# Kernel optimization log

Hardware: AMD Instinct MI355X
Metric: run time of the kernel (lower is better)

The kernel has to match this reference:

```python
import jax, jax.numpy as jnp
import numpy as np

D_MODEL = 1024
N_EXPERTS = 16
TOP_K = 2
D_FF = 512      # per-expert SwiGLU hidden size
D_FF_SHARED = 1024
N_TOKENS = 4096


def setup_inputs() -> dict:
    key = jax.random.key(0)
    ks = jax.random.split(key, 9)
    s_in = 1.0 / np.sqrt(D_MODEL)
    s_ff = 1.0 / np.sqrt(D_FF)
    s_fs = 1.0 / np.sqrt(D_FF_SHARED)
    return {
        "hidden_states": jax.random.normal(ks[0], (N_TOKENS, D_MODEL), jnp.float32),
        "Wg": jax.random.normal(ks[1], (D_MODEL, N_EXPERTS), jnp.float32) * s_in,
        "w1": jax.random.normal(ks[2], (N_EXPERTS, D_MODEL, D_FF), jnp.float32) * s_in,
        "w3": jax.random.normal(ks[3], (N_EXPERTS, D_MODEL, D_FF), jnp.float32) * s_in,
        "w2": jax.random.normal(ks[4], (N_EXPERTS, D_FF, D_MODEL), jnp.float32) * s_ff,
        "ws1": jax.random.normal(ks[5], (D_MODEL, D_FF_SHARED), jnp.float32) * s_in,
        "ws3": jax.random.normal(ks[6], (D_MODEL, D_FF_SHARED), jnp.float32) * s_in,
        "ws2": jax.random.normal(ks[7], (D_FF_SHARED, D_MODEL), jnp.float32) * s_fs,
        "capacity": 1024,
    }


def reference(hidden_states, Wg, w1, w3, w2, ws1, ws3, ws2, capacity):
    T, d = hidden_states.shape
    E = Wg.shape[1]
    C = capacity

    # --- router: softmax in fp32, top-k, renormalize (norm_topk_prob=True) ---
    logits = hidden_states @ Wg                                  # [T, E]
    probs = jax.nn.softmax(logits.astype(jnp.float32), axis=-1)
    topw, topi = jax.lax.top_k(probs, TOP_K)                     # [T, K]
    topw = topw / jnp.sum(topw, axis=-1, keepdims=True)
    topw = topw.astype(hidden_states.dtype)

    # --- dispatch: flatten (token, k) pairs, compute slot within expert buffer ---
    flat_e = topi.reshape(-1)                                    # [T*K] expert id
    flat_t = jnp.repeat(jnp.arange(T), TOP_K)                    # [T*K] source token
    flat_w = topw.reshape(-1)                                    # [T*K]
    oh = jax.nn.one_hot(flat_e, E, dtype=jnp.int32)              # [T*K, E]
    # exclusive position of each pair within its expert's buffer
    pos = jnp.sum((jnp.cumsum(oh, axis=0) - 1) * oh, axis=-1)    # [T*K]
    keep = pos < C
    slot = jnp.where(keep, flat_e * C + pos, E * C)              # dropped -> dummy row

    buf = jnp.zeros((E * C + 1, d), hidden_states.dtype)
    buf = buf.at[slot].set(hidden_states[flat_t])
    xb = buf[: E * C].reshape(E, C, d)                           # [E, C, d]

    # --- per-expert SwiGLU MLP (grouped matmuls) ---
    h = jax.nn.silu(jnp.einsum("ecd,edf->ecf", xb, w1)) * jnp.einsum("ecd,edf->ecf", xb, w3)
    ob = jnp.einsum("ecf,efd->ecd", h, w2).reshape(E * C, d)     # [E*C, d]

    # --- weighted combine: gather expert outputs, scatter-add into token rows ---
    gathered = ob[jnp.minimum(slot, E * C - 1)]                  # [T*K, d]
    y = gathered * (flat_w * keep.astype(flat_w.dtype))[:, None]
    final = jnp.zeros_like(hidden_states).at[flat_t].add(y)

    # --- shared expert (dense SwiGLU over all tokens) ---
    sh = jax.nn.silu(hidden_states @ ws1) * (hidden_states @ ws3)
    final = final + sh @ ws2
    return final
```

## Files before the change

kernel.cpp:

```cpp
#include <hip/hip_runtime.h>
#include <stdint.h>

#define TT 4096
#define DM 1024
#define NE 16
#define DFF 512
#define DFS 1024
#define CAP 1024

typedef unsigned short u16;
typedef __bf16 bf16x8 __attribute__((ext_vector_type(8)));
typedef float f32x4 __attribute__((ext_vector_type(4)));

typedef __attribute__((address_space(1))) void as1_void;
typedef __attribute__((address_space(3))) void as3_void;

__device__ __forceinline__ u16 f2bf(float f) {
  union { float f; uint32_t u; } v; v.f = f;
  uint32_t u = v.u;
  u += 0x7fffu + ((u >> 16) & 1u);
  return (u16)(u >> 16);
}

__device__ __forceinline__ float bf2f(u16 b) {
  union { uint32_t u; float f; } v; v.u = ((uint32_t)b) << 16;
  return v.f;
}

__device__ __forceinline__ void gl2lds16(const void* g, void* l) {
  __builtin_amdgcn_global_load_lds(
      (as1_void*)(uintptr_t)g,
      (as3_void*)(uint32_t)(uintptr_t)l,
      16, 0, 0);
}

__global__ __launch_bounds__(256) void k_prep(
    const float* __restrict__ x, const float* __restrict__ Wg,
    const float* __restrict__ w1, const float* __restrict__ w3,
    const float* __restrict__ w2, const float* __restrict__ ws1,
    const float* __restrict__ ws3, const float* __restrict__ ws2,
    u16* __restrict__ hbf,
    u16* __restrict__ w1t, u16* __restrict__ w3t, u16* __restrict__ w2t,
    u16* __restrict__ ws1t, u16* __restrict__ ws3t, u16* __restrict__ ws2t,
    int* __restrict__ counts, int* __restrict__ tok_slot,
    int* __restrict__ tslot, float* __restrict__ tw) {
  __shared__ __align__(16) char smraw[18496];
  __shared__ int pick_e[32];
  __shared__ int base_sh[16];
  const int bid = blockIdx.x;
  const int tid = threadIdx.x;

  if (bid < 256) {
    float (*red)[16][17] = (float(*)[16][17])smraw;
    float (*lg)[17] = (float(*)[17])(smraw + 17408);
    int tl = tid >> 4, kp = tid & 15;
    int t = bid * 16 + tl;
    const float* xr = x + (size_t)t * DM + kp * 64;
    u16* hr = hbf + (size_t)t * DM + kp * 64;
    float acc[16];
#pragma unroll
    for (int e = 0; e < 16; ++e) acc[e] = 0.f;
#pragma unroll 4
    for (int i = 0; i < 16; ++i) {
      float4 xv = *(const float4*)(xr + i * 4);
      ushort4 o;
      o.x = f2bf(xv.x); o.y = f2bf(xv.y); o.z = f2bf(xv.z); o.w = f2bf(xv.w);
      *(ushort4*)(hr + i * 4) = o;
      const float* wgr = Wg + (size_t)(kp * 64 + i * 4) * NE;
#pragma unroll
      for (int q = 0; q < 4; ++q) {
        float xq = (q == 0) ? xv.x : (q == 1) ? xv.y : (q == 2) ? xv.z : xv.w;
        float4 a = *(const float4*)(wgr + q * NE);
        float4 b = *(const float4*)(wgr + q * NE + 4);
        float4 c = *(const float4*)(wgr + q * NE + 8);
        float4 d = *(const float4*)(wgr + q * NE + 12);
        acc[0] += xq * a.x;  acc[1] += xq * a.y;  acc[2] += xq * a.z;  acc[3] += xq * a.w;
        acc[4] += xq * b.x;  acc[5] += xq * b.y;  acc[6] += xq * b.z;  acc[7] += xq * b.w;
        acc[8] += xq * c.x;  acc[9] += xq * c.y;  acc[10] += xq * c.z; acc[11] += xq * c.w;
        acc[12] += xq * d.x; acc[13] += xq * d.y; acc[14] += xq * d.z; acc[15] += xq * d.w;
      }
    }
#pragma unroll
    for (int e = 0; e < 16; ++e) red[tl][kp][e] = acc[e];
    __syncthreads();
    float logit = 0.f;
#pragma unroll
    for (int p = 0; p < 16; ++p) logit += red[tl][p][kp];
    lg[tl][kp] = logit;
    __syncthreads();
    if (kp == 0) {
      float b0 = -1e30f; int i0 = 0;
#pragma unroll
      for (int i = 0; i < NE; ++i) { float v = lg[tl][i]; if (v > b0) { b0 = v; i0 = i; } }
      float b1 = -1e30f; int i1 = 0;
#pragma unroll
      for (int i = 0; i < NE; ++i) { if (i == i0) continue; float v = lg[tl][i]; if (v > b1) { b1 = v; i1 = i; } }
      float ex = __expf(b1 - b0);
      float w0 = 1.f / (1.f + ex);
      float w1v = 1.f - w0;
      pick_e[2 * tl] = i0;
      pick_e[2 * tl + 1] = i1;
      tw[2 * t] = w0; tw[2 * t + 1] = w1v;
    }
    __syncthreads();
    if (tid < 16) {
      int c = 0;
#pragma unroll
      for (int j = 0; j < 32; ++j) c += (pick_e[j] == tid) ? 1 : 0;
      int base = 0;
      if (c > 0) base = atomicAdd(&counts[tid], c);
      base_sh[tid] = base;
    }
    __syncthreads();
    if (kp == 0) {
#pragma unroll
      for (int kk = 0; kk < 2; ++kk) {
        int idx = 2 * tl + kk;
        int e = pick_e[idx];
        int rank = 0;
        for (int j = 0; j < idx; ++j) rank += (pick_e[j] == e) ? 1 : 0;
        int p = base_sh[e] + rank;
        int s = -1;
        if (p < CAP) { s = e * CAP + p; tok_slot[s] = t; }
        tslot[2 * t + kk] = s;
      }
    }
    return;
  }

  int tb = bid - 256;
  int z = tb >> 8, xy = tb & 255;
  const float* ip; u16* op; int R, C;
  if (z < 16)      { ip = w1 + (size_t)z * DM * DFF;       op = w1t + (size_t)z * DM * DFF;       R = DM;  C = DFF; }
  else if (z < 32) { int e = z - 16; ip = w3 + (size_t)e * DM * DFF; op = w3t + (size_t)e * DM * DFF; R = DM;  C = DFF; }
  else if (z < 48) { int e = z - 32; ip = w2 + (size_t)e * DFF * DM; op = w2t + (size_t)e * DFF * DM; R = DFF; C = DM; }
  else if (z == 48){ ip = ws1; op = ws1t; R = DM;  C = DFS; }
  else if (z == 49){ ip = ws3; op = ws3t; R = DM;  C = DFS; }
  else             { ip = ws2; op = ws2t; R = DFS; C = DM; }

  int c0 = (xy & 15) * 64, r0 = (xy >> 4) * 64;
  if (c0 >= C || r0 >= R) return;

  float (*tile)[65] = (float(*)[65])smraw;
  int tx = tid & 15, ty = tid >> 4;
#pragma unroll
  for (int j = 0; j < 4; ++j) {
    int r = ty + 16 * j;
    float4 v = *(const float4*)&ip[(size_t)(r0 + r) * C + c0 + tx * 4];
    *(float4*)&tile[r][tx * 4] = v;
  }
  __syncthreads();
#pragma unroll
  for (int j = 0; j < 4; ++j) {
    int c = ty + 16 * j;
    ushort4 o;
    o.x = f2bf(tile[tx * 4 + 0][c]);
    o.y = f2bf(tile[tx * 4 + 1][c]);
    o.z = f2bf(tile[tx * 4 + 2][c]);
    o.w = f2bf(tile[tx * 4 + 3][c]);
    *(ushort4*)&op[(size_t)(c0 + c) * R + r0 + tx * 4] = o;
  }
}

#define FRAG(BUF, ROW, CC)                                                       \
  (*(const bf16x8*)&BUF[(ROW) * 64 + ((((CC) * 4 + lq) ^ ((ROW) & 7)) << 3)])

__global__ __launch_bounds__(128) void k_up(
    const u16* __restrict__ hbf,
    const u16* __restrict__ ws1t, const u16* __restrict__ ws3t,
    const u16* __restrict__ w1t, const u16* __restrict__ w3t,
    u16* __restrict__ hs, u16* __restrict__ hexp,
    const int* __restrict__ counts, const int* __restrict__ tok_slot) {
  const int bid = blockIdx.x;
  const int tid = threadIdx.x;
  const u16* B1p; const u16* B3p; u16* Cp;
  int m0, n0, N;
  int e = -1, cnt = 0;
  if (bid < 512) {
    m0 = (bid >> 4) * 128; n0 = (bid & 15) * 64;
    B1p = ws1t; B3p = ws3t; Cp = hs; N = DFS;
  } else {
    int r = bid - 512;
    e = r >> 6; int q = r & 63;
    m0 = (q >> 3) * 128; n0 = (q & 7) * 64;
    cnt = counts[e]; if (cnt > CAP) cnt = CAP;
    if (m0 >= cnt) return;
    B1p = w1t + (size_t)e * (DFF * DM);
    B3p = w3t + (size_t)e * (DFF * DM);
    Cp = hexp + (size_t)e * (CAP * DFF);
    N = DFF;
  }

  __shared__ __align__(16) u16 As[128 * 64];
  __shared__ __align__(16) u16 Bs1[64 * 64];
  __shared__ __align__(16) u16 Bs3[64 * 64];

  uint32_t aoff[8], boff[4];
#pragma unroll
  for (int j = 0; j < 8; ++j) {
    int L = tid + 128 * j;
    int row = L >> 3;
    int c = (L & 7) ^ (row & 7);
    int gr;
    if (e >= 0) {
      int rr = m0 + row;
      gr = (rr < cnt) ? tok_slot[e * CAP + rr] : 0;
    } else {
      gr = m0 + row;
    }
    aoff[j] = (uint32_t)gr * DM + c * 8;
  }
#pragma unroll
  for (int j = 0; j < 4; ++j) {
    int L = tid + 128 * j;
    int row = L >> 3;
    int c = (L & 7) ^ (row & 7);
    boff[j] = (uint32_t)(n0 + row) * DM + c * 8;
  }

  const int lane = tid & 63;
  const int wv = tid >> 6;
  const int wr = wv * 64;
  const int lr = lane & 15;
  const int lq = lane >> 4;

  f32x4 acc1[4][4], acc3[4][4];
#pragma unroll
  for (int i = 0; i < 4; ++i)
#pragma unroll
    for (int j = 0; j < 4; ++j) {
      acc1[i][j] = (f32x4){0.f, 0.f, 0.f, 0.f};
      acc3[i][j] = (f32x4){0.f, 0.f, 0.f, 0.f};
    }

  for (int k0 = 0; k0 < DM; k0 += 64) {
    __syncthreads();
#pragma unroll
    for (int j = 0; j < 8; ++j) gl2lds16(hbf + aoff[j] + k0, &As[(size_t)(tid + 128 * j) * 8]);
#pragma unroll
    for (int j = 0; j < 4; ++j) gl2lds16(B1p + boff[j] + k0, &Bs1[(size_t)(tid + 128 * j) * 8]);
#pragma unroll
    for (int j = 0; j < 4; ++j) gl2lds16(B3p + boff[j] + k0, &Bs3[(size_t)(tid + 128 * j) * 8]);
    __syncthreads();
#pragma unroll
    for (int cc = 0; cc < 2; ++cc) {
      bf16x8 af[4], bf1[4], bf3[4];
#pragma unroll
      for (int i = 0; i < 4; ++i) af[i] = FRAG(As, wr + i * 16 + lr, cc);
#pragma unroll
      for (int j = 0; j < 4; ++j) {
        bf1[j] = FRAG(Bs1, j * 16 + lr, cc);
        bf3[j] = FRAG(Bs3, j * 16 + lr, cc);
      }
#pragma unroll
      for (int i = 0; i < 4; ++i)
#pragma unroll
        for (int j = 0; j < 4; ++j) {
          acc1[i][j] = __builtin_amdgcn_mfma_f32_16x16x32_bf16(af[i], bf1[j], acc1[i][j], 0, 0, 0);
          acc3[i][j] = __builtin_amdgcn_mfma_f32_16x16x32_bf16(af[i], bf3[j], acc3[i][j], 0, 0, 0);
        }
    }
  }

#pragma unroll
  for (int i = 0; i < 4; ++i)
#pragma unroll
    for (int r = 0; r < 4; ++r) {
      int row = m0 + wr + i * 16 + lq * 4 + r;
      u16* crow = Cp + (size_t)row * N;
#pragma unroll
      for (int j = 0; j < 4; ++j) {
        float v1 = acc1[i][j][r];
        float v3 = acc3[i][j][r];
        float h = (v1 / (1.f + __expf(-v1))) * v3;
        crow[n0 + j * 16 + lr] = f2bf(h);
      }
    }
}

__global__ __launch_bounds__(128) void k_down(
    const u16* __restrict__ hs, const u16* __restrict__ ws2t,
    const u16* __restrict__ hexp, const u16* __restrict__ w2t,
    float* __restrict__ out, u16* __restrict__ ob,
    const int* __restrict__ counts) {
  const int bid = blockIdx.x;
  const int tid = threadIdx.x;
  const u16* Ap; const u16* Bp;
  int m0, n0, K, e = -1;
  if (bid < 512) {
    m0 = (bid >> 4) * 128; n0 = (bid & 15) * 64;
    Ap = hs; Bp = ws2t; K = DFS;
  } else {
    int r = bid - 512;
    e = r >> 7; int q = r & 127;
    m0 = (q >> 4) * 128; n0 = (q & 15) * 64;
    int cnt = counts[e]; if (cnt > CAP) cnt = CAP;
    if (m0 >= cnt) return;
    Ap = hexp + (size_t)e * (CAP * DFF);
    Bp = w2t + (size_t)e * (DM * DFF);
    K = DFF;
  }

  __shared__ __align__(16) u16 As[128 * 64];
  __shared__ __align__(16) u16 Bs[64 * 64];

  uint32_t aoff[8], boff[4];
#pragma unroll
  for (int j = 0; j < 8; ++j) {
    int L = tid + 128 * j;
    int row = L >> 3;
    int c = (L & 7) ^ (row & 7);
    aoff[j] = (uint32_t)(m0 + row) * K + c * 8;
  }
#pragma unroll
  for (int j = 0; j < 4; ++j) {
    int L = tid + 128 * j;
    int row = L >> 3;
    int c = (L & 7) ^ (row & 7);
    boff[j] = (uint32_t)(n0 + row) * K + c * 8;
  }

  const int lane = tid & 63;
  const int wv = tid >> 6;
  const int wr = wv * 64;
  const int lr = lane & 15;
  const int lq = lane >> 4;

  f32x4 acc[4][4];
#pragma unroll
  for (int i = 0; i < 4; ++i)
#pragma unroll
    for (int j = 0; j < 4; ++j) acc[i][j] = (f32x4){0.f, 0.f, 0.f, 0.f};

  for (int k0 = 0; k0 < K; k0 += 64) {
    __syncthreads();
#pragma unroll
    for (int j = 0; j < 8; ++j) gl2lds16(Ap + aoff[j] + k0, &As[(size_t)(tid + 128 * j) * 8]);
#pragma unroll
    for (int j = 0; j < 4; ++j) gl2lds16(Bp + boff[j] + k0, &Bs[(size_t)(tid + 128 * j) * 8]);
    __syncthreads();
#pragma unroll
    for (int cc = 0; cc < 2; ++cc) {
      bf16x8 af[4], bfr[4];
#pragma unroll
      for (int i = 0; i < 4; ++i) af[i] = FRAG(As, wr + i * 16 + lr, cc);
#pragma unroll
      for (int j = 0; j < 4; ++j) bfr[j] = FRAG(Bs, j * 16 + lr, cc);
#pragma unroll
      for (int i = 0; i < 4; ++i)
#pragma unroll
        for (int j = 0; j < 4; ++j)
          acc[i][j] = __builtin_amdgcn_mfma_f32_16x16x32_bf16(af[i], bfr[j], acc[i][j], 0, 0, 0);
    }
  }

  if (e < 0) {
#pragma unroll
    for (int i = 0; i < 4; ++i)
#pragma unroll
      for (int r = 0; r < 4; ++r) {
        int row = m0 + wr + i * 16 + lq * 4 + r;
        float* orow = out + (size_t)row * DM;
#pragma unroll
        for (int j = 0; j < 4; ++j)
          orow[n0 + j * 16 + lr] = acc[i][j][r];
      }
  } else {
    u16* obase = ob + (size_t)e * CAP * DM;
#pragma unroll
    for (int i = 0; i < 4; ++i)
#pragma unroll
      for (int r = 0; r < 4; ++r) {
        int row = m0 + wr + i * 16 + lq * 4 + r;
        u16* orow = obase + (size_t)row * DM;
#pragma unroll
        for (int j = 0; j < 4; ++j)
          orow[n0 + j * 16 + lr] = f2bf(acc[i][j][r]);
      }
  }
}

__global__ __launch_bounds__(256) void k_combine(
    float* __restrict__ out, const u16* __restrict__ ob,
    const int* __restrict__ tslot, const float* __restrict__ tw) {
  int t = blockIdx.x;
  int c = threadIdx.x * 4;
  int s0 = tslot[2 * t], s1 = tslot[2 * t + 1];
  float w0 = tw[2 * t], w1 = tw[2 * t + 1];
  float4 v = *(float4*)&out[(size_t)t * DM + c];
  if (s0 >= 0) {
    ushort4 o = *(const ushort4*)&ob[(size_t)s0 * DM + c];
    v.x += w0 * bf2f(o.x); v.y += w0 * bf2f(o.y);
    v.z += w0 * bf2f(o.z); v.w += w0 * bf2f(o.w);
  }
  if (s1 >= 0) {
    ushort4 o = *(const ushort4*)&ob[(size_t)s1 * DM + c];
    v.x += w1 * bf2f(o.x); v.y += w1 * bf2f(o.y);
    v.z += w1 * bf2f(o.z); v.w += w1 * bf2f(o.w);
  }
  *(float4*)&out[(size_t)t * DM + c] = v;
}

extern "C" void kernel_launch(void* const* d_in, const int* in_sizes, int n_in,
                              void* d_out, int out_size, void* d_ws, size_t ws_size,
                              hipStream_t stream) {
  (void)in_sizes; (void)n_in; (void)out_size; (void)ws_size;
  const float* x   = (const float*)d_in[0];
  const float* Wg  = (const float*)d_in[1];
  const float* w1  = (const float*)d_in[2];
  const float* w3  = (const float*)d_in[3];
  const float* w2  = (const float*)d_in[4];
  const float* ws1 = (const float*)d_in[5];
  const float* ws3 = (const float*)d_in[6];
  const float* ws2 = (const float*)d_in[7];
  float* out = (float*)d_out;
  char* ws = (char*)d_ws;

  u16* hbf   = (u16*)(ws + 0);
  u16* w1t   = (u16*)(ws + 8388608);
  u16* w3t   = (u16*)(ws + 25165824);
  u16* w2t   = (u16*)(ws + 41943040);
  u16* ws1t  = (u16*)(ws + 58720256);
  u16* ws3t  = (u16*)(ws + 60817408);
  u16* ws2t  = (u16*)(ws + 62914560);
  u16* hs    = (u16*)(ws + 65011712);
  u16* hexp  = (u16*)(ws + 73400320);
  int* counts    = (int*)(ws + 90177536);
  int* tok_slot  = (int*)(ws + 90177792);
  int* tslot     = (int*)(ws + 90243328);
  float* tw      = (float*)(ws + 90276096);
  u16* ob    = (u16*)(ws + 0);

  hipMemsetAsync(counts, 0, NE * sizeof(int), stream);

  k_prep<<<dim3(256 + 51 * 256), dim3(256), 0, stream>>>(
      x, Wg, w1, w3, w2, ws1, ws3, ws2,
      hbf, w1t, w3t, w2t, ws1t, ws3t, ws2t,
      counts, tok_slot, tslot, tw);

  k_up<<<dim3(512 + NE * 64), dim3(128), 0, stream>>>(
      hbf, ws1t, ws3t, w1t, w3t, hs, hexp, counts, tok_slot);

  k_down<<<dim3(512 + NE * 128), dim3(128), 0, stream>>>(
      hs, ws2t, hexp, w2t, out, ob, counts);

  k_combine<<<dim3(TT), dim3(256), 0, stream>>>(out, ob, tslot, tw);
}
```

Before: 319.9 us.

## Double-buffer LDS tiles in up and down expert GEMM kernels

Both the gate/up GEMM and the down GEMM now keep two LDS buffers per operand. The next K tile's global-to-LDS loads are issued before computing on the current tile, so memory latency overlaps MFMA work and one barrier per iteration is removed. This doubles shared memory use, which may cut occupancy: the up kernel grows to 64KB, the down kernel to 48KB. Correctness relies on gl2lds16 completing before the following barrier.

```diff
diff --git a/kernel.cpp b/kernel.cpp
--- a/kernel.cpp
+++ b/kernel.cpp
@@ -191,9 +191,9 @@
     N = DFF;
   }
 
-  __shared__ __align__(16) u16 As[128 * 64];
-  __shared__ __align__(16) u16 Bs1[64 * 64];
-  __shared__ __align__(16) u16 Bs3[64 * 64];
+  __shared__ __align__(16) u16 As[2][128 * 64];
+  __shared__ __align__(16) u16 Bs1[2][64 * 64];
+  __shared__ __align__(16) u16 Bs3[2][64 * 64];
 
   uint32_t aoff[8], boff[4];
 #pragma unroll
@@ -233,34 +233,55 @@
       acc3[i][j] = (f32x4){0.f, 0.f, 0.f, 0.f};
     }
 
-  for (int k0 = 0; k0 < DM; k0 += 64) {
-    __syncthreads();
-#pragma unroll
-    for (int j = 0; j < 8; ++j) gl2lds16(hbf + aoff[j] + k0, &As[(size_t)(tid + 128 * j) * 8]);
-#pragma unroll
-    for (int j = 0; j < 4; ++j) gl2lds16(B1p + boff[j] + k0, &Bs1[(size_t)(tid + 128 * j) * 8]);
-#pragma unroll
-    for (int j = 0; j < 4; ++j) gl2lds16(B3p + boff[j] + k0, &Bs3[(size_t)(tid + 128 * j) * 8]);
-    __syncthreads();
-#pragma unroll
-    for (int cc = 0; cc < 2; ++cc) {
-      bf16x8 af[4], bf1[4], bf3[4];
-#pragma unroll
-      for (int i = 0; i < 4; ++i) af[i] = FRAG(As, wr + i * 16 + lr, cc);
-#pragma unroll
-      for (int j = 0; j < 4; ++j) {
-        bf1[j] = FRAG(Bs1, j * 16 + lr, cc);
-        bf3[j] = FRAG(Bs3, j * 16 + lr, cc);
-      }
-#pragma unroll
-      for (int i = 0; i < 4; ++i)
-#pragma unroll
-        for (int j = 0; j < 4; ++j) {
-          acc1[i][j] = __builtin_amdgcn_mfma_f32_16x16x32_bf16(af[i], bf1[j], acc1[i][j], 0, 0, 0);
-          acc3[i][j] = __builtin_amdgcn_mfma_f32_16x16x32_bf16(af[i], bf3[j], acc3[i][j], 0, 0, 0);
-        }
-    }
-  }
+#define UP_STAGE(B, K0)                                                              \
+  do {                                                                               \
+    _Pragma("unroll")                                                                \
+    for (int j = 0; j < 8; ++j)                                                      \
+      gl2lds16(hbf + aoff[j] + (K0), &As[B][(size_t)(tid + 128 * j) * 8]);           \
+    _Pragma("unroll")                                                                \
+    for (int j = 0; j < 4; ++j)                                                      \
+      gl2lds16(B1p + boff[j] + (K0), &Bs1[B][(size_t)(tid + 128 * j) * 8]);          \
+    _Pragma("unroll")                                                                \
+    for (int j = 0; j < 4; ++j)                                                      \
+      gl2lds16(B3p + boff[j] + (K0), &Bs3[B][(size_t)(tid + 128 * j) * 8]);          \
+  } while (0)
+
+#define UP_COMPUTE(B)                                                                \
+  do {                                                                               \
+    const u16* Ab = &As[B][0];                                                       \
+    const u16* B1b = &Bs1[B][0];                                                     \
+    const u16* B3b = &Bs3[B][0];                                                     \
+    _Pragma("unroll")                                                                \
+    for (int cc = 0; cc < 2; ++cc) {                                                 \
+      bf16x8 af[4], bf1[4], bf3[4];                                                  \
+      _Pragma("unroll")                                                              \
+      for (int i = 0; i < 4; ++i) af[i] = FRAG(Ab, wr + i * 16 + lr, cc);            \
+      _Pragma("unroll")                                                              \
+      for (int j = 0; j < 4; ++j) {                                                  \
+        bf1[j] = FRAG(B1b, j * 16 + lr, cc);                                         \
+        bf3[j] = FRAG(B3b, j * 16 + lr, cc);                                         \
+      }                                                                              \
+      _Pragma("unroll")                                                              \
+      for (int i = 0; i < 4; ++i)                                                    \
+        _Pragma("unroll")                                                            \
+        for (int j = 0; j < 4; ++j) {                                                \
+          acc1[i][j] = __builtin_amdgcn_mfma_f32_16x16x32_bf16(af[i], bf1[j], acc1[i][j], 0, 0, 0); \
+          acc3[i][j] = __builtin_amdgcn_mfma_f32_16x16x32_bf16(af[i], bf3[j], acc3[i][j], 0, 0, 0); \
+        }                                                                            \
+    }                                                                                \
+  } while (0)
+
+  UP_STAGE(0, 0);
+  __syncthreads();
+  int cur = 0;
+  const int NT = DM / 64;
+  for (int t = 0; t < NT - 1; ++t) {
+    UP_STAGE(cur ^ 1, (t + 1) * 64);
+    UP_COMPUTE(cur);
+    __syncthreads();
+    cur ^= 1;
+  }
+  UP_COMPUTE(cur);
 
 #pragma unroll
   for (int i = 0; i < 4; ++i)
@@ -301,8 +322,8 @@
     K = DFF;
   }
 
-  __shared__ __align__(16) u16 As[128 * 64];
-  __shared__ __align__(16) u16 Bs[64 * 64];
+  __shared__ __align__(16) u16 As[2][128 * 64];
+  __shared__ __align__(16) u16 Bs[2][64 * 64];
 
   uint32_t aoff[8], boff[4];
 #pragma unroll
@@ -332,27 +353,46 @@
 #pragma unroll
     for (int j = 0; j < 4; ++j) acc[i][j] = (f32x4){0.f, 0.f, 0.f, 0.f};
 
-  for (int k0 = 0; k0 < K; k0 += 64) {
-    __syncthreads();
-#pragma unroll
-    for (int j = 0; j < 8; ++j) gl2lds16(Ap + aoff[j] + k0, &As[(size_t)(tid + 128 * j) * 8]);
-#pragma unroll
-    for (int j = 0; j < 4; ++j) gl2lds16(Bp + boff[j] + k0, &Bs[(size_t)(tid + 128 * j) * 8]);
-    __syncthreads();
-#pragma unroll
-    for (int cc = 0; cc < 2; ++cc) {
-      bf16x8 af[4], bfr[4];
-#pragma unroll
-      for (int i = 0; i < 4; ++i) af[i] = FRAG(As, wr + i * 16 + lr, cc);
-#pragma unroll
-      for (int j = 0; j < 4; ++j) bfr[j] = FRAG(Bs, j * 16 + lr, cc);
-#pragma unroll
-      for (int i = 0; i < 4; ++i)
-#pragma unroll
-        for (int j = 0; j < 4; ++j)
-          acc[i][j] = __builtin_amdgcn_mfma_f32_16x16x32_bf16(af[i], bfr[j], acc[i][j], 0, 0, 0);
-    }
-  }
+#define DN_STAGE(B, K0)                                                              \
+  do {                                                                               \
+    _Pragma("unroll")                                                                \
+    for (int j = 0; j < 8; ++j)                                                      \
+      gl2lds16(Ap + aoff[j] + (K0), &As[B][(size_t)(tid + 128 * j) * 8]);            \
+    _Pragma("unroll")                                                                \
+    for (int j = 0; j < 4; ++j)                                                      \
+      gl2lds16(Bp + boff[j] + (K0), &Bs[B][(size_t)(tid + 128 * j) * 8]);            \
+  } while (0)
+
+#define DN_COMPUTE(B)                                                                \
+  do {                                                                               \
+    const u16* Ab = &As[B][0];                                                       \
+    const u16* Bb = &Bs[B][0];                                                       \
+    _Pragma("unroll")                                                                \
+    for (int cc = 0; cc < 2; ++cc) {                                                 \
+      bf16x8 af[4], bfr[4];                                                          \
+      _Pragma("unroll")                                                              \
+      for (int i = 0; i < 4; ++i) af[i] = FRAG(Ab, wr + i * 16 + lr, cc);            \
+      _Pragma("unroll")                                                              \
+      for (int j = 0; j < 4; ++j) bfr[j] = FRAG(Bb, j * 16 + lr, cc);                \
+      _Pragma("unroll")                                                              \
+      for (int i = 0; i < 4; ++i)                                                    \
+        _Pragma("unroll")                                                            \
+        for (int j = 0; j < 4; ++j)                                                  \
+          acc[i][j] = __builtin_amdgcn_mfma_f32_16x16x32_bf16(af[i], bfr[j], acc[i][j], 0, 0, 0); \
+    }                                                                                \
+  } while (0)
+
+  DN_STAGE(0, 0);
+  __syncthreads();
+  int cur = 0;
+  const int NT = K / 64;
+  for (int t = 0; t < NT - 1; ++t) {
+    DN_STAGE(cur ^ 1, (t + 1) * 64);
+    DN_COMPUTE(cur);
+    __syncthreads();
+    cur ^= 1;
+  }
+  DN_COMPUTE(cur);
 
   if (e < 0) {
 #pragma unroll
```

After: 311.1 us. 1.03x faster.
